# Kernel tuning notes

Measured on AMD Instinct MI355X. Metric: run time of the kernel, lower is better.

## Reference

```python
import jax, jax.numpy as jnp
import numpy as np

DEPTH = 3
UNITS = 512
INNER = 32          # inner_dim == F-1
F = INNER + 1
B, N = 128, 100


def setup_inputs() -> dict:
    key = jax.random.key(0)
    k1, k2, k3, k4, k5 = jax.random.split(key, 5)
    x = jax.random.normal(k1, (B, N, N, F), dtype=jnp.float32)
    # W_inner: identity tiled + small uniform noise (init_inner='identity')
    W_inner = (jnp.tile(jnp.eye(INNER, dtype=jnp.float32)[None], (DEPTH + 1, 1, 1))
               + jax.random.uniform(k2, (DEPTH + 1, INNER, INNER), minval=-0.05, maxval=0.05))
    b_inner = jax.random.uniform(k3, (DEPTH + 1, 1, INNER), minval=-0.05, maxval=0.05)
    # W_output: uniform with scale_output=0.01, tiled across depths; b_output zeros
    W_out_single = jax.random.uniform(k4, (INNER, UNITS), minval=-0.01, maxval=0.01)
    W_output = jnp.tile(W_out_single[None], (DEPTH + 1, 1, 1))
    b_output = jnp.zeros((DEPTH + 1, 1, UNITS), dtype=jnp.float32)
    return {"x": x, "W_inner": W_inner, "b_inner": b_inner,
            "W_output": W_output, "b_output": b_output}


def _fp_contribution(attr, W_output, b_output, d):
    # softmax over the units axis, per atom; attr[:, :-1] is [N, INNER]
    return jax.nn.softmax(attr[:, :-1] @ W_output[d] + b_output[d, 0], axis=-1)


def _single(graph0, W_inner, b_inner, W_output, b_output):
    # graph0: [N, N, F]
    attr = jnp.diagonal(graph0, axis1=0, axis2=1).T            # [N, F]
    fp = _fp_contribution(attr, W_output, b_output, 0).sum(axis=0)
    bonds = graph0[:, :, -1]                                    # [N, N]
    boa_T = (bonds + jnp.eye(bonds.shape[0], dtype=graph0.dtype)).T  # bonds_or_atoms transposed: [i,j]=boa[j,i]
    graph = graph0
    for d in range(1, DEPTH + 1):
        pre = graph.sum(axis=1)                                 # [N, F] row-sums of each feature slice
        core = pre[:, :-1] @ W_inner[d] + b_inner[d, 0]         # linear inner activation
        new_attr = jnp.concatenate([core, attr[:, -1:]], axis=1)  # keep bond channel
        # graph[i,j,f] += boa[j,i] * (new_attr - attr)[i,f]  (rank-1 per atom)
        graph = graph + boa_T[:, :, None] * (new_attr - attr)[:, None, :]
        attr = new_attr
        fp = fp + _fp_contribution(attr, W_output, b_output, d).sum(axis=0)
    return fp


def reference(x, W_inner, b_inner, W_output, b_output):
    return jax.vmap(lambda g: _single(g, W_inner, b_inner, W_output, b_output))(x)  # [B, UNITS]
```

## Files before the change

kernel.cpp:

```cpp
#include <hip/hip_runtime.h>

typedef __attribute__((ext_vector_type(4))) float f32x4;
typedef __attribute__((ext_vector_type(8))) short s16x8;

#define NB 128
#define NA 100
#define KF 32
#define NF 33
#define NU 512
#define ND 3
#define LOG2E 1.4426950408889634f

#define SZ_S0    (NB * NA * KF)
#define SZ_BONDS (NB * NA * NA)

#define EXP2F(x) __builtin_amdgcn_exp2f(x)
#define LOG2F(x) __builtin_amdgcn_logf(x)

__device__ __forceinline__ unsigned short f2bf(float f) {
    unsigned int u = __float_as_uint(f);
    u = (u + 0x7fffu + ((u >> 16) & 1u)) >> 16;
    return (unsigned short)u;
}
__device__ __forceinline__ float bf2f(unsigned short h) {
    return __uint_as_float(((unsigned int)h) << 16);
}
__device__ __forceinline__ unsigned int pack_bf16(float a, float b) {
    const unsigned int ua = (__float_as_uint(a) + 0x8000u) >> 16;
    const unsigned int ub = (__float_as_uint(b) + 0x8000u) & 0xffff0000u;
    return ua | ub;
}

__global__ __launch_bounds__(256) void p1_reduce(const float* __restrict__ x,
    float* __restrict__ S0, float* __restrict__ attrAll, float* __restrict__ bonds)
{
    const int blk = blockIdx.x;
    const int b   = blk / NA;
    const int i   = blk % NA;
    const int t   = threadIdx.x;

    __shared__ float lds[NA * NF];
    __shared__ float red[8][KF];

    const float4* row4 = (const float4*)(x + (size_t)blk * (NA * NF));
    float4* lds4 = (float4*)lds;
    for (int idx = t; idx < (NA * NF) / 4; idx += 256) lds4[idx] = row4[idx];
    __syncthreads();

    const int g = t >> 5;
    const int f = t & 31;
    float p0 = 0.f, p1 = 0.f;
    for (int j = g; j + 8 < NA; j += 16) {
        p0 += lds[j * NF + f];
        p1 += lds[(j + 8) * NF + f];
    }
    if (g < 4) p0 += lds[(96 + g) * NF + f];
    red[g][f] = p0 + p1;
    __syncthreads();

    if (t < KF) {
        float s = 0.f;
#pragma unroll
        for (int gg = 0; gg < 8; ++gg) s += red[gg][t];
        S0[(size_t)blk * KF + t] = s;
    } else if (t >= 64 && t < 64 + KF) {
        attrAll[(size_t)b * (ND + 1) * NA * KF + (size_t)i * KF + (t - 64)] = lds[i * NF + (t - 64)];
    } else if (t >= 128 && t < 128 + NA) {
        const int j = t - 128;
        bonds[(size_t)blk * NA + j] = lds[j * NF + KF];
    }
}

#define NAH 50
#define ELH (NAH * KF)
__global__ __launch_bounds__(256) void p2a_recur(
    const float* __restrict__ S0, const float* __restrict__ bonds,
    const float* __restrict__ W_inner, const float* __restrict__ b_inner,
    float* __restrict__ attrAll,
    const float* __restrict__ W_output,
    unsigned short* __restrict__ WBh, unsigned short* __restrict__ WBl)
{
    const int blk = blockIdx.x;
    const int t   = threadIdx.x;

    if (blk >= NB * 2) {
        const int pb = blk - NB * 2;
        const int base = pb * 4096;
        for (int j = t; j < 4096; j += 256) {
            const int i = base + j;
            const int d = i >> 14, rem = i & 16383, k = rem >> 9, col = rem & 511;
            const float v = W_output[(size_t)d * (KF * NU) + (size_t)k * NU + col] * LOG2E;
            const unsigned short hi = f2bf(v);
            const unsigned short lo = f2bf(v - bf2f(hi));
            const int dst = d * 16384 + (col >> 4) * 512 + (k >> 3) * 128 + (col & 15) * 8 + (k & 7);
            WBh[dst] = hi;
            WBl[dst] = lo;
        }
        return;
    }

    __shared__ float S[ELH];
    __shared__ float attr[ELH];
    __shared__ float rs[NAH];

    const int half = blk & 1;
    const int b    = blk >> 1;
    const int f    = t & 31;

    const float4* s4 = (const float4*)(S0 + (size_t)b * NA * KF + half * ELH);
    const float4* a4 = (const float4*)(attrAll + (size_t)b * (ND + 1) * NA * KF + half * ELH);
    for (int idx = t; idx < ELH / 4; idx += 256) {
        ((float4*)S)[idx]    = s4[idx];
        ((float4*)attr)[idx] = a4[idx];
    }
    if (t < NAH) {
        const int i = half * NAH + t;
        const float* bb = bonds + (size_t)b * NA * NA + i;
        float c0=0.f,c1=0.f,c2=0.f,c3=0.f,c4=0.f,c5=0.f,c6=0.f,c7=0.f;
        int j = 0;
        for (; j + 8 <= NA; j += 8) {
            c0 += bb[(j+0)*NA]; c1 += bb[(j+1)*NA];
            c2 += bb[(j+2)*NA]; c3 += bb[(j+3)*NA];
            c4 += bb[(j+4)*NA]; c5 += bb[(j+5)*NA];
            c6 += bb[(j+6)*NA]; c7 += bb[(j+7)*NA];
        }
        for (; j < NA; ++j) c0 += bb[j*NA];
        rs[t] = 1.f + (((c0+c1)+(c2+c3))+((c4+c5)+(c6+c7)));
    }
    __syncthreads();

    float* attrDst = attrAll + (size_t)b * (ND + 1) * NA * KF + half * ELH;

    for (int d = 1; d <= ND; ++d) {
        float Wc[KF];
        const float* Wd = W_inner + d * KF * KF + f;
#pragma unroll
        for (int k = 0; k < KF; ++k) Wc[k] = Wd[k * KF];
        const float bi = b_inner[d * KF + f];

        float core[7];
#pragma unroll
        for (int it = 0; it < 7; ++it) {
            const int idx = t + it * 256;
            if (idx < ELH) {
                const int row = idx >> 5;
                const float4* Sr4 = (const float4*)(S + row * KF);
                float acc = bi;
#pragma unroll
                for (int q = 0; q < 8; ++q) {
                    const float4 sv = Sr4[q];
                    acc += sv.x * Wc[4*q] + sv.y * Wc[4*q+1]
                         + sv.z * Wc[4*q+2] + sv.w * Wc[4*q+3];
                }
                core[it] = acc;
            }
        }
        __syncthreads();
#pragma unroll
        for (int it = 0; it < 7; ++it) {
            const int idx = t + it * 256;
            if (idx < ELH) {
                const int row = idx >> 5;
                const float cc  = core[it];
                const float old = attr[idx];
                attr[idx] = cc;
                S[idx] += rs[row] * (cc - old);
                attrDst[(size_t)d * NA * KF + idx] = cc;
            }
        }
        __syncthreads();
    }
}

__global__ __launch_bounds__(448, 4) void p2b_mfma(
    const float* __restrict__ attrAll,
    const unsigned short* __restrict__ WBh_g, const unsigned short* __restrict__ WBl_g,
    const float* __restrict__ b_output, float* __restrict__ fpPart)
{
    extern __shared__ unsigned char smraw[];
    unsigned short* WBh  = (unsigned short*)smraw;
    unsigned short* aAh  = WBh + 16384;
    unsigned short* aAl  = aAh + 3584;
    float*          biasL= (float*)(aAl + 3584);
    float*          fpw  = (float*)aAh;

    const int blk = blockIdx.x;
    const int b   = blk & (NB - 1);
    const int d   = blk >> 7;
    const int t   = threadIdx.x;
    const int l   = t & 63;
    const int w   = t >> 6;

    for (int i = t; i < 2048; i += 448) ((float4*)WBh)[i] = ((const float4*)WBh_g)[d * 2048 + i];
    for (int i = t; i < NU; i += 448)   biasL[i] = b_output[d * NU + i] * LOG2E;

    const float* A = attrAll + ((size_t)b * (ND + 1) + d) * (NA * KF);
    for (int i = t; i < 3584; i += 448) {
        const int gr = i >> 5, k = i & 31;
        const float v = (gr < NA) ? A[gr * KF + k] : 0.f;
        const unsigned short hi = f2bf(v);
        const unsigned short lo = f2bf(v - bf2f(hi));
        const int dst = ((gr >> 4) * 4 + (k >> 3)) * 128 + (gr & 15) * 8 + (k & 7);
        aAh[dst] = hi;
        aAl[dst] = lo;
    }
    __syncthreads();

    const int aoff = (w * 4 + (l >> 4)) * 128 + (l & 15) * 8;
    const s16x8 ah = *(const s16x8*)&aAh[aoff];
    const s16x8 al = *(const s16x8*)&aAl[aoff];
    __syncthreads();

    const int laneoff = (l >> 4) * 128 + (l & 15) * 8;
    const unsigned short* wblg = WBl_g + d * 16384;
    const f32x4 z = {0.f, 0.f, 0.f, 0.f};

    float m[4] = {-1e30f, -1e30f, -1e30f, -1e30f};
#pragma unroll 4
    for (int tt = 0; tt < 32; ++tt) {
        const s16x8 bh = *(const s16x8*)&WBh[tt * 512 + laneoff];
        const f32x4 c = __builtin_amdgcn_mfma_f32_16x16x32_bf16(ah, bh, z, 0, 0, 0);
        const float bias = biasL[tt * 16 + (l & 15)];
#pragma unroll
        for (int r = 0; r < 4; ++r) m[r] = fmaxf(m[r], c[r] + bias);
    }
#pragma unroll
    for (int off = 1; off <= 8; off <<= 1)
#pragma unroll
        for (int r = 0; r < 4; ++r) m[r] = fmaxf(m[r], __shfl_xor(m[r], off, 64));

    float s[4] = {0.f, 0.f, 0.f, 0.f};
#pragma unroll 2
    for (int tt = 0; tt < 16; ++tt) {
        const s16x8 bh = *(const s16x8*)&WBh[tt * 512 + laneoff];
        const s16x8 bl = *(const s16x8*)&wblg[tt * 512 + laneoff];
        f32x4 c = __builtin_amdgcn_mfma_f32_16x16x32_bf16(ah, bh, z, 0, 0, 0);
        c = __builtin_amdgcn_mfma_f32_16x16x32_bf16(ah, bl, c, 0, 0, 0);
        c = __builtin_amdgcn_mfma_f32_16x16x32_bf16(al, bh, c, 0, 0, 0);
        const float bias = biasL[tt * 16 + (l & 15)];
#pragma unroll
        for (int r = 0; r < 4; ++r)
            s[r] += EXP2F(c[r] + bias - m[r]);
    }

    unsigned int eP[32];
#pragma unroll
    for (int tt = 16; tt < 32; ++tt) {
        const s16x8 bh = *(const s16x8*)&WBh[tt * 512 + laneoff];
        const s16x8 bl = *(const s16x8*)&wblg[tt * 512 + laneoff];
        f32x4 c = __builtin_amdgcn_mfma_f32_16x16x32_bf16(ah, bh, z, 0, 0, 0);
        c = __builtin_amdgcn_mfma_f32_16x16x32_bf16(ah, bl, c, 0, 0, 0);
        c = __builtin_amdgcn_mfma_f32_16x16x32_bf16(al, bh, c, 0, 0, 0);
        const float bias = biasL[tt * 16 + (l & 15)];
        const float e0 = EXP2F(c[0] + bias - m[0]);
        const float e1 = EXP2F(c[1] + bias - m[1]);
        const float e2 = EXP2F(c[2] + bias - m[2]);
        const float e3 = EXP2F(c[3] + bias - m[3]);
        s[0] += e0; s[1] += e1; s[2] += e2; s[3] += e3;
        eP[(tt - 16) * 2]     = pack_bf16(e0, e1);
        eP[(tt - 16) * 2 + 1] = pack_bf16(e2, e3);
    }
#pragma unroll
    for (int off = 1; off <= 8; off <<= 1)
#pragma unroll
        for (int r = 0; r < 4; ++r) s[r] += __shfl_xor(s[r], off, 64);

    float K[4], inv[4];
#pragma unroll
    for (int r = 0; r < 4; ++r) {
        const int grow = w * 16 + (l >> 4) * 4 + r;
        const bool ok = (grow < NA);
        K[r]   = ok ? (m[r] + LOG2F(s[r])) : 1e30f;
        inv[r] = ok ? (1.f / s[r]) : 0.f;
    }

#pragma unroll 2
    for (int tt = 0; tt < 16; ++tt) {
        const s16x8 bh = *(const s16x8*)&WBh[tt * 512 + laneoff];
        const s16x8 bl = *(const s16x8*)&wblg[tt * 512 + laneoff];
        f32x4 c = __builtin_amdgcn_mfma_f32_16x16x32_bf16(ah, bh, z, 0, 0, 0);
        c = __builtin_amdgcn_mfma_f32_16x16x32_bf16(ah, bl, c, 0, 0, 0);
        c = __builtin_amdgcn_mfma_f32_16x16x32_bf16(al, bh, c, 0, 0, 0);
        const float bias = biasL[tt * 16 + (l & 15)];
        float f = 0.f;
#pragma unroll
        for (int r = 0; r < 4; ++r)
            f += EXP2F(c[r] + bias - K[r]);
        f += __shfl_xor(f, 16, 64);
        f += __shfl_xor(f, 32, 64);
        if (l < 16) fpw[w * NU + tt * 16 + l] = f;
    }
#pragma unroll
    for (int tt = 16; tt < 32; ++tt) {
        const unsigned int p01 = eP[(tt - 16) * 2];
        const unsigned int p23 = eP[(tt - 16) * 2 + 1];
        float f = __uint_as_float(p01 << 16)         * inv[0]
                + __uint_as_float(p01 & 0xffff0000u) * inv[1]
                + __uint_as_float(p23 << 16)         * inv[2]
                + __uint_as_float(p23 & 0xffff0000u) * inv[3];
        f += __shfl_xor(f, 16, 64);
        f += __shfl_xor(f, 32, 64);
        if (l < 16) fpw[w * NU + tt * 16 + l] = f;
    }
    __syncthreads();

    for (int u = t; u < NU; u += 448) {
        float sacc = 0.f;
#pragma unroll
        for (int ww = 0; ww < 7; ++ww) sacc += fpw[ww * NU + u];
        fpPart[((size_t)d * NB + b) * NU + u] = sacc;
    }
}

__global__ __launch_bounds__(512) void p2c_out(const float* __restrict__ fpPart,
                                               float* __restrict__ out)
{
    const int b = blockIdx.x, t = threadIdx.x;
    float s = 0.f;
#pragma unroll
    for (int d = 0; d <= ND; ++d) s += fpPart[((size_t)d * NB + b) * NU + t];
    out[(size_t)b * NU + t] = s;
}

extern "C" void kernel_launch(void* const* d_in, const int* in_sizes, int n_in,
                              void* d_out, int out_size, void* d_ws, size_t ws_size,
                              hipStream_t stream) {
    (void)in_sizes; (void)n_in; (void)out_size; (void)ws_size;
    const float* x        = (const float*)d_in[0];
    const float* W_inner  = (const float*)d_in[1];
    const float* b_inner  = (const float*)d_in[2];
    const float* W_output = (const float*)d_in[3];
    const float* b_output = (const float*)d_in[4];
    float* out = (float*)d_out;

    float* S0      = (float*)d_ws;
    float* bonds   = S0 + SZ_S0;
    float* attrAll = bonds + SZ_BONDS;
    unsigned short* WBh = (unsigned short*)(attrAll + (size_t)NB * (ND + 1) * NA * KF);
    unsigned short* WBl = WBh + 65536;
    float* fpPart = bonds;

    p1_reduce<<<NB * NA, 256, 0, stream>>>(x, S0, attrAll, bonds);
    p2a_recur<<<NB * 2 + 16, 256, 0, stream>>>(S0, bonds, W_inner, b_inner, attrAll,
                                               W_output, WBh, WBl);

    const size_t smemB = 49152;
    hipFuncSetAttribute(reinterpret_cast<const void*>(p2b_mfma),
                        hipFuncAttributeMaxDynamicSharedMemorySize, (int)smemB);
    p2b_mfma<<<NB * (ND + 1), 448, smemB, stream>>>(attrAll, WBh, WBl, b_output, fpPart);
    p2c_out<<<NB, 512, 0, stream>>>(fpPart, out);
}
```

Before: 67.57 us.

## Fuse row-reduction kernel into recurrence kernel and drop S0/bonds intermediates

```diff
diff --git a/kernel.cpp b/kernel.cpp
--- a/kernel.cpp
+++ b/kernel.cpp
@@ -10,9 +10,9 @@
 #define NU 512
 #define ND 3
 #define LOG2E 1.4426950408889634f
-
-#define SZ_S0    (NB * NA * KF)
-#define SZ_BONDS (NB * NA * NA)
+#define NAH 50
+#define ELH (NAH * KF)
+#define TPB 512
 
 #define EXP2F(x) __builtin_amdgcn_exp2f(x)
 #define LOG2F(x) __builtin_amdgcn_logf(x)
@@ -31,50 +31,8 @@
     return ua | ub;
 }
 
-__global__ __launch_bounds__(256) void p1_reduce(const float* __restrict__ x,
-    float* __restrict__ S0, float* __restrict__ attrAll, float* __restrict__ bonds)
-{
-    const int blk = blockIdx.x;
-    const int b   = blk / NA;
-    const int i   = blk % NA;
-    const int t   = threadIdx.x;
-
-    __shared__ float lds[NA * NF];
-    __shared__ float red[8][KF];
-
-    const float4* row4 = (const float4*)(x + (size_t)blk * (NA * NF));
-    float4* lds4 = (float4*)lds;
-    for (int idx = t; idx < (NA * NF) / 4; idx += 256) lds4[idx] = row4[idx];
-    __syncthreads();
-
-    const int g = t >> 5;
-    const int f = t & 31;
-    float p0 = 0.f, p1 = 0.f;
-    for (int j = g; j + 8 < NA; j += 16) {
-        p0 += lds[j * NF + f];
-        p1 += lds[(j + 8) * NF + f];
-    }
-    if (g < 4) p0 += lds[(96 + g) * NF + f];
-    red[g][f] = p0 + p1;
-    __syncthreads();
-
-    if (t < KF) {
-        float s = 0.f;
-#pragma unroll
-        for (int gg = 0; gg < 8; ++gg) s += red[gg][t];
-        S0[(size_t)blk * KF + t] = s;
-    } else if (t >= 64 && t < 64 + KF) {
-        attrAll[(size_t)b * (ND + 1) * NA * KF + (size_t)i * KF + (t - 64)] = lds[i * NF + (t - 64)];
-    } else if (t >= 128 && t < 128 + NA) {
-        const int j = t - 128;
-        bonds[(size_t)blk * NA + j] = lds[j * NF + KF];
-    }
-}
-
-#define NAH 50
-#define ELH (NAH * KF)
-__global__ __launch_bounds__(256) void p2a_recur(
-    const float* __restrict__ S0, const float* __restrict__ bonds,
+__global__ __launch_bounds__(TPB) void p12a(
+    const float* __restrict__ x,
     const float* __restrict__ W_inner, const float* __restrict__ b_inner,
     float* __restrict__ attrAll,
     const float* __restrict__ W_output,
@@ -86,7 +44,7 @@
     if (blk >= NB * 2) {
         const int pb = blk - NB * 2;
         const int base = pb * 4096;
-        for (int j = t; j < 4096; j += 256) {
+        for (int j = t; j < 4096; j += TPB) {
             const int i = base + j;
             const int d = i >> 14, rem = i & 16383, k = rem >> 9, col = rem & 511;
             const float v = W_output[(size_t)d * (KF * NU) + (size_t)k * NU + col] * LOG2E;
@@ -99,37 +57,65 @@
         return;
     }
 
+    __shared__ float lds[NA * NF];
+    __shared__ float red[16 * KF];
     __shared__ float S[ELH];
     __shared__ float attr[ELH];
     __shared__ float rs[NAH];
 
     const int half = blk & 1;
     const int b    = blk >> 1;
-    const int f    = t & 31;
-
-    const float4* s4 = (const float4*)(S0 + (size_t)b * NA * KF + half * ELH);
-    const float4* a4 = (const float4*)(attrAll + (size_t)b * (ND + 1) * NA * KF + half * ELH);
-    for (int idx = t; idx < ELH / 4; idx += 256) {
-        ((float4*)S)[idx]    = s4[idx];
-        ((float4*)attr)[idx] = a4[idx];
-    }
+
+    if (t < NAH) rs[t] = 1.f;
+
+    for (int u = 0; u < NAH; ++u) {
+        const int i = half * NAH + u;
+        const float4* row4 = (const float4*)(x + ((size_t)b * NA + i) * (NA * NF));
+        __syncthreads();
+        for (int idx = t; idx < (NA * NF) / 4; idx += TPB) ((float4*)lds)[idx] = row4[idx];
+        __syncthreads();
+
+        const int g = t >> 5;
+        const int f = t & 31;
+        float p = 0.f;
+        for (int j = g; j < NA; j += 16) p += lds[j * NF + f];
+        red[g * KF + f] = p;
+        __syncthreads();
+
+        if (t < KF) {
+            float s = 0.f;
+#pragma unroll
+            for (int gg = 0; gg < 16; ++gg) s += red[gg * KF + t];
+            S[u * KF + t] = s;
+        } else if (t >= 64 && t < 64 + KF) {
+            const int k = t - 64;
+            const float v = lds[i * NF + k];
+            attr[u * KF + k] = v;
+            attrAll[(size_t)b * (ND + 1) * NA * KF + (size_t)i * KF + k] = v;
+        }
+        if (t < NAH) rs[t] += lds[(half * NAH + t) * NF + KF];
+    }
+
     if (t < NAH) {
-        const int i = half * NAH + t;
-        const float* bb = bonds + (size_t)b * NA * NA + i;
+        const int col = half * NAH + t;
+        const float* xb = x + ((size_t)b * NA + (size_t)(1 - half) * NAH) * (NA * NF)
+                            + (size_t)col * NF + KF;
+        const size_t stride = (size_t)NA * NF;
         float c0=0.f,c1=0.f,c2=0.f,c3=0.f,c4=0.f,c5=0.f,c6=0.f,c7=0.f;
         int j = 0;
-        for (; j + 8 <= NA; j += 8) {
-            c0 += bb[(j+0)*NA]; c1 += bb[(j+1)*NA];
-            c2 += bb[(j+2)*NA]; c3 += bb[(j+3)*NA];
-            c4 += bb[(j+4)*NA]; c5 += bb[(j+5)*NA];
-            c6 += bb[(j+6)*NA]; c7 += bb[(j+7)*NA];
-        }
-        for (; j < NA; ++j) c0 += bb[j*NA];
-        rs[t] = 1.f + (((c0+c1)+(c2+c3))+((c4+c5)+(c6+c7)));
+        for (; j + 8 <= NAH; j += 8) {
+            c0 += xb[(j+0)*stride]; c1 += xb[(j+1)*stride];
+            c2 += xb[(j+2)*stride]; c3 += xb[(j+3)*stride];
+            c4 += xb[(j+4)*stride]; c5 += xb[(j+5)*stride];
+            c6 += xb[(j+6)*stride]; c7 += xb[(j+7)*stride];
+        }
+        for (; j < NAH; ++j) c0 += xb[j*stride];
+        rs[t] += (((c0+c1)+(c2+c3))+((c4+c5)+(c6+c7)));
     }
     __syncthreads();
 
     float* attrDst = attrAll + (size_t)b * (ND + 1) * NA * KF + half * ELH;
+    const int f = t & 31;
 
     for (int d = 1; d <= ND; ++d) {
         float Wc[KF];
@@ -138,10 +124,10 @@
         for (int k = 0; k < KF; ++k) Wc[k] = Wd[k * KF];
         const float bi = b_inner[d * KF + f];
 
-        float core[7];
-#pragma unroll
-        for (int it = 0; it < 7; ++it) {
-            const int idx = t + it * 256;
+        float core[4];
+#pragma unroll
+        for (int it = 0; it < 4; ++it) {
+            const int idx = t + it * TPB;
             if (idx < ELH) {
                 const int row = idx >> 5;
                 const float4* Sr4 = (const float4*)(S + row * KF);
@@ -157,8 +143,8 @@
         }
         __syncthreads();
 #pragma unroll
-        for (int it = 0; it < 7; ++it) {
-            const int idx = t + it * 256;
+        for (int it = 0; it < 4; ++it) {
+            const int idx = t + it * TPB;
             if (idx < ELH) {
                 const int row = idx >> 5;
                 const float cc  = core[it];
@@ -333,16 +319,13 @@
     const float* b_output = (const float*)d_in[4];
     float* out = (float*)d_out;
 
-    float* S0      = (float*)d_ws;
-    float* bonds   = S0 + SZ_S0;
-    float* attrAll = bonds + SZ_BONDS;
-    unsigned short* WBh = (unsigned short*)(attrAll + (size_t)NB * (ND + 1) * NA * KF);
+    float* attrAll = (float*)d_ws;
+    float* fpPart  = attrAll + (size_t)NB * (ND + 1) * NA * KF;
+    unsigned short* WBh = (unsigned short*)(fpPart + (size_t)(ND + 1) * NB * NU);
     unsigned short* WBl = WBh + 65536;
-    float* fpPart = bonds;
-
-    p1_reduce<<<NB * NA, 256, 0, stream>>>(x, S0, attrAll, bonds);
-    p2a_recur<<<NB * 2 + 16, 256, 0, stream>>>(S0, bonds, W_inner, b_inner, attrAll,
-                                               W_output, WBh, WBl);
+
+    p12a<<<NB * 2 + 16, TPB, 0, stream>>>(x, W_inner, b_inner, attrAll,
+                                          W_output, WBh, WBl);
 
     const size_t smemB = 49152;
     hipFuncSetAttribute(reinterpret_cast<const void*>(p2b_mfma),
```

New measurement: 105.1 us. +55.6%, slower.
